# Optimization experiments

Hardware: AMD Instinct MI355X
Metric: run time of the kernel (lower is better)

Reference implementation:

```python
import jax, jax.numpy as jnp
import numpy as np

W, HN, C, NHEAD = 256, 128, 512, 8


def layer_norm(x, w, b, eps=1e-5):
    m = x.mean(-1, keepdims=True)
    v = ((x - m) ** 2).mean(-1, keepdims=True)
    return (x - m) / jnp.sqrt(v + eps) * w + b


def setup_inputs() -> dict:
    key = jax.random.key(0)
    ks = jax.random.split(key, 6)
    s = 0.02
    return {
        "feat_left": jax.random.normal(ks[0], (W, HN, C), jnp.float32),
        "feat_right": jax.random.normal(ks[1], (W, HN, C), jnp.float32),
        "pos": jax.random.normal(ks[2], (2 * W - 1, C), jnp.float32),
        "pos_indexes": jax.random.randint(ks[3], (W * W,), 0, 2 * W - 1, dtype=jnp.int32),
        "ln_w": jnp.ones((C,), jnp.float32),
        "ln_b": jnp.zeros((C,), jnp.float32),
        "in_proj_w": jax.random.normal(ks[4], (3 * C, C), jnp.float32) * s,
        "in_proj_b": jnp.zeros((3 * C,), jnp.float32),
        "out_w": jax.random.normal(ks[5], (C, C), jnp.float32) * s,
        "out_b": jnp.zeros((C,), jnp.float32),
    }


def reference(feat_left, feat_right, pos, pos_indexes, ln_w, ln_b, in_proj_w, in_proj_b, out_w, out_b):
    w, n, c = feat_left.shape
    e = NHEAD
    hd = c // e
    scaling = hd ** -0.5

    # pre-norm (same norm1 applied to both streams)
    ql = layer_norm(feat_left, ln_w, ln_b)     # [W,N,C]
    kv_in = layer_norm(feat_right, ln_w, ln_b)  # [W,N,C]

    # cross-attn projections: q from left with in_proj[:C], k/v from right with in_proj[C:]
    q = ql @ in_proj_w[:c].T + in_proj_b[:c]
    kv = kv_in @ in_proj_w[c:].T + in_proj_b[c:]
    k, v = jnp.split(kv, 2, axis=-1)

    # relative pos encoding gather: [2W-1,C] -> [W*W,C] -> [W,W',C]
    pe = pos[pos_indexes].reshape(w, w, c)
    qr_kr = pe @ in_proj_w[: 2 * c].T + in_proj_b[: 2 * c]
    q_r, k_r = jnp.split(qr_kr, 2, axis=-1)

    q = (q * scaling).reshape(w, n, e, hd)
    q_r = (q_r * scaling).reshape(w, w, e, hd)
    k = k.reshape(w, n, e, hd)
    v = v.reshape(w, n, e, hd)
    k_r = k_r.reshape(w, w, e, hd)

    # content-content + content-pos + pos-content scores: [N,E,W,W']
    attn = (jnp.einsum('wnec,vnec->newv', q, k)
            + jnp.einsum('wnec,wvec->newv', q, k_r)
            + jnp.einsum('vnec,wvec->newv', k, q_r))

    raw_attn = attn.sum(axis=1)                      # [N,W,W']
    p = jax.nn.softmax(attn, axis=-1)
    v_o = jnp.einsum('newv,vnec->wnec', p, v).reshape(w, n, c)
    v_o = v_o @ out_w.T + out_b

    return feat_left + v_o, raw_attn
```

## Files before the change

### kernel.cpp

```cpp
#include <hip/hip_runtime.h>

#define WW 256
#define NB 128
#define CD 512
#define NE 8
#define HD 64
#define NCHUNKS 4
#define SCALING 0.125f

typedef __attribute__((ext_vector_type(8))) short bfx8;
typedef __attribute__((ext_vector_type(4))) float fx4;

#define OFF_MEAN   0u
#define OFF_RSTD   65536u
#define OFF_WPB    131072u
#define OFF_OWB    524288u
#define OFF_S      655360u
#define OFF_U      656896u
#define OFF_PQ     658432u
#define OFF_PK     789504u
#define OFF_QB     920576u
#define OFF_KB     9309184u
#define OFF_VB     17697792u
#define OFF_ATTN   26086400u
#define OFF_T3     42863616u
#define OFF_PB     51252224u
#define OFF_VOB    59640832u

__device__ __forceinline__ unsigned short f2bf(float f) {
  unsigned u = __builtin_bit_cast(unsigned, f);
  u = (u + 0x7fffu + ((u >> 16) & 1u)) >> 16;
  return (unsigned short)u;
}
__device__ __forceinline__ float bf2f(unsigned short h) {
  unsigned u = ((unsigned)h) << 16;
  return __builtin_bit_cast(float, u);
}

#define GLDS16(g, l)                                                          \
  __builtin_amdgcn_global_load_lds(                                           \
      (const __attribute__((address_space(1))) void*)(g),                     \
      (__attribute__((address_space(3))) void*)(l), 16, 0, 0)

__global__ __launch_bounds__(256) void cvt_kernel(const float* __restrict__ a,
                                                  unsigned short* __restrict__ b,
                                                  int n8) {
  int i = blockIdx.x * 256 + threadIdx.x;
  if (i >= n8) return;
  float4 x = ((const float4*)a)[2 * i];
  float4 y = ((const float4*)a)[2 * i + 1];
  int4 o;
  o.x = (int)(((unsigned)f2bf(x.y) << 16) | f2bf(x.x));
  o.y = (int)(((unsigned)f2bf(x.w) << 16) | f2bf(x.z));
  o.z = (int)(((unsigned)f2bf(y.y) << 16) | f2bf(y.x));
  o.w = (int)(((unsigned)f2bf(y.w) << 16) | f2bf(y.z));
  ((int4*)b)[i] = o;
}

__global__ __launch_bounds__(256) void stats_kernel(const float* __restrict__ L,
                                                    const float* __restrict__ R,
                                                    float* __restrict__ mean,
                                                    float* __restrict__ rstd,
                                                    unsigned short* __restrict__ flb,
                                                    unsigned short* __restrict__ frb) {
  int wave = threadIdx.x >> 6, lane = threadIdx.x & 63;
  int row = blockIdx.x * 4 + wave;
  const float* src = (row < 32768) ? (L + (size_t)row * CD) : (R + (size_t)(row - 32768) * CD);
  unsigned short* drow = (row < 32768) ? (flb + (size_t)row * CD) : (frb + (size_t)(row - 32768) * CD);
  float4 a = *(const float4*)(src + lane * 4);
  float4 b = *(const float4*)(src + 256 + lane * 4);
  short4 sa, sb;
  sa.x = (short)f2bf(a.x); sa.y = (short)f2bf(a.y); sa.z = (short)f2bf(a.z); sa.w = (short)f2bf(a.w);
  sb.x = (short)f2bf(b.x); sb.y = (short)f2bf(b.y); sb.z = (short)f2bf(b.z); sb.w = (short)f2bf(b.w);
  *(short4*)(drow + lane * 4) = sa;
  *(short4*)(drow + 256 + lane * 4) = sb;
  float s  = a.x + a.y + a.z + a.w + b.x + b.y + b.z + b.w;
  float ss = a.x*a.x + a.y*a.y + a.z*a.z + a.w*a.w + b.x*b.x + b.y*b.y + b.z*b.z + b.w*b.w;
#pragma unroll
  for (int off = 32; off > 0; off >>= 1) {
    s  += __shfl_xor(s, off);
    ss += __shfl_xor(ss, off);
  }
  if (lane == 0) {
    float m = s * (1.0f / 512.0f);
    float v = ss * (1.0f / 512.0f) - m * m;
    mean[row] = m;
    rstd[row] = rsqrtf(v + 1e-5f);
  }
}

__global__ __launch_bounds__(256) void prep_kernel(const float* __restrict__ ipw,
                                                   const float* __restrict__ ipb,
                                                   const float* __restrict__ lnw,
                                                   const float* __restrict__ lnb,
                                                   unsigned short* __restrict__ Wpb,
                                                   float* __restrict__ S,
                                                   float* __restrict__ U) {
  int o = blockIdx.x, t = threadIdx.x;
  float s = 0.f, u = 0.f;
#pragma unroll
  for (int j0 = 0; j0 < 512; j0 += 256) {
    int j = j0 + t;
    float w0 = ipw[(size_t)o * 512 + j];
    float wl = w0 * lnw[j];
    unsigned short h = f2bf(wl);
    Wpb[(size_t)o * 512 + j] = h;
    s += bf2f(h);
    u += w0 * lnb[j];
  }
  __shared__ float rs[4], ru[4];
  int lane = t & 63, wv = t >> 6;
#pragma unroll
  for (int off = 32; off > 0; off >>= 1) { s += __shfl_xor(s, off); u += __shfl_xor(u, off); }
  if (lane == 0) { rs[wv] = s; ru[wv] = u; }
  __syncthreads();
  if (t == 0) {
    S[o] = rs[0] + rs[1] + rs[2] + rs[3];
    U[o] = ru[0] + ru[1] + ru[2] + ru[3] + ipb[o];
  }
}

__global__ __launch_bounds__(256) void gemm_ln(const unsigned short* __restrict__ A,
                                               const unsigned short* __restrict__ Bw,
                                               const float* __restrict__ S,
                                               const float* __restrict__ U,
                                               const float* __restrict__ mean,
                                               const float* __restrict__ rstd,
                                               unsigned short* __restrict__ out0,
                                               unsigned short* __restrict__ out1,
                                               int wOff, int statOff, float scale) {
  __shared__ unsigned short As[2][128 * 32];
  __shared__ unsigned short Bs[2][128 * 32];
  int t = threadIdx.x;
  int lane = t & 63, w = t >> 6;
  int quad = lane >> 4, l15 = lane & 15;
  int wm = w >> 1, wn = w & 1;
  int m0 = blockIdx.x * 128, n0 = blockIdx.y * 128;

  int cs = ((lane & 3) ^ ((lane >> 3) & 3)) * 8;
  unsigned lo0 = (unsigned)(w * 16) * 32;
  unsigned lo1 = (unsigned)(64 + w * 16) * 32;
  const unsigned short* gA0 = A + (size_t)(m0 + w * 16 + (lane >> 2)) * 512 + cs;
  const unsigned short* gA1 = gA0 + (size_t)64 * 512;
  const unsigned short* gB0 = Bw + (size_t)(wOff + n0 + w * 16 + (lane >> 2)) * 512 + cs;
  const unsigned short* gB1 = gB0 + (size_t)64 * 512;

  fx4 acc[4][4];
#pragma unroll
  for (int i = 0; i < 4; ++i)
#pragma unroll
    for (int j = 0; j < 4; ++j) acc[i][j] = (fx4){0.f, 0.f, 0.f, 0.f};

  int ro = (quad ^ ((l15 >> 1) & 3)) * 8;

#define STAGE_G(buf, kk)                                                      \
  do {                                                                        \
    GLDS16(gA0 + (kk), &As[buf][lo0]);                                        \
    GLDS16(gA1 + (kk), &As[buf][lo1]);                                        \
    GLDS16(gB0 + (kk), &Bs[buf][lo0]);                                        \
    GLDS16(gB1 + (kk), &Bs[buf][lo1]);                                        \
  } while (0)

#define COMPUTE_G(buf)                                                        \
  do {                                                                        \
    const unsigned short* Ab = &As[buf][0];                                   \
    const unsigned short* Bb = &Bs[buf][0];                                   \
    bfx8 af[4], bfr[4];                                                       \
    _Pragma("unroll")                                                         \
    for (int i = 0; i < 4; ++i)                                               \
      af[i] = *(const bfx8*)(Ab + (size_t)(wm * 64 + i * 16 + l15) * 32 + ro);\
    _Pragma("unroll")                                                         \
    for (int j = 0; j < 4; ++j)                                               \
      bfr[j] = *(const bfx8*)(Bb + (size_t)(wn * 64 + j * 16 + l15) * 32 + ro);\
    _Pragma("unroll")                                                         \
    for (int i = 0; i < 4; ++i)                                               \
      _Pragma("unroll")                                                       \
      for (int j = 0; j < 4; ++j)                                             \
        acc[i][j] = __builtin_amdgcn_mfma_f32_16x16x32_bf16(af[i], bfr[j], acc[i][j], 0, 0, 0); \
  } while (0)

  STAGE_G(0, 0);
  int cur = 0;
  for (int kt = 0; kt < 480; kt += 32) {
    STAGE_G(cur ^ 1, kt + 32);
    asm volatile("s_waitcnt vmcnt(4)" ::: "memory");
    __builtin_amdgcn_s_barrier();
    __builtin_amdgcn_sched_barrier(0);
    COMPUTE_G(cur);
    asm volatile("s_waitcnt lgkmcnt(0)" ::: "memory");
    __builtin_amdgcn_s_barrier();
    __builtin_amdgcn_sched_barrier(0);
    cur ^= 1;
  }
  asm volatile("s_waitcnt vmcnt(0)" ::: "memory");
  __builtin_amdgcn_s_barrier();
  __builtin_amdgcn_sched_barrier(0);
  COMPUTE_G(cur);

  float mn[16], rs[16];
#pragma unroll
  for (int i = 0; i < 4; ++i)
#pragma unroll
    for (int r = 0; r < 4; ++r) {
      int m = statOff + m0 + wm * 64 + i * 16 + quad * 4 + r;
      mn[i * 4 + r] = mean[m];
      rs[i * 4 + r] = rstd[m];
    }
#pragma unroll
  for (int j = 0; j < 4; ++j) {
    int oc = n0 + wn * 64 + j * 16 + l15;
    int o = wOff + oc;
    float Sv = S[o], Uv = U[o];
    unsigned short* dst; int cc;
    if (oc < 512) { dst = out0; cc = oc; } else { dst = out1; cc = oc - 512; }
#pragma unroll
    for (int i = 0; i < 4; ++i)
#pragma unroll
      for (int r = 0; r < 4; ++r) {
        int m = m0 + wm * 64 + i * 16 + quad * 4 + r;
        dst[(size_t)m * 512 + cc] =
            f2bf(((acc[i][j][r] - mn[i * 4 + r] * Sv) * rs[i * 4 + r] + Uv) * scale);
      }
  }
#undef STAGE_G
#undef COMPUTE_G
}

__global__ __launch_bounds__(256) void gemm_out(const unsigned short* __restrict__ A,
                                                const unsigned short* __restrict__ Bw,
                                                const float* __restrict__ ob,
                                                const float* __restrict__ fl,
                                                float* __restrict__ out, int wc) {
  __shared__ unsigned short As[2][128 * 32];
  __shared__ unsigned short Bs[2][128 * 32];
  int t = threadIdx.x;
  int lane = t & 63, w = t >> 6;
  int quad = lane >> 4, l15 = lane & 15;
  int wm = w >> 1, wn = w & 1;
  int n0 = blockIdx.x * 128, m0 = blockIdx.y * 128;

  int cs = ((lane & 3) ^ ((lane >> 3) & 3)) * 8;
  unsigned lo0 = (unsigned)(w * 16) * 32;
  unsigned lo1 = (unsigned)(64 + w * 16) * 32;
  const unsigned short* gA0 = A + (size_t)(m0 + w * 16 + (lane >> 2)) * 512 + cs;
  const unsigned short* gA1 = gA0 + (size_t)64 * 512;
  const unsigned short* gB0 = Bw + (size_t)(n0 + w * 16 + (lane >> 2)) * 512 + cs;
  const unsigned short* gB1 = gB0 + (size_t)64 * 512;

  fx4 acc[4][4];
#pragma unroll
  for (int i = 0; i < 4; ++i)
#pragma unroll
    for (int j = 0; j < 4; ++j) acc[i][j] = (fx4){0.f, 0.f, 0.f, 0.f};

  int ro = (quad ^ ((l15 >> 1) & 3)) * 8;

#define STAGE_O(buf, kk)                                                      \
  do {                                                                        \
    GLDS16(gA0 + (kk), &As[buf][lo0]);                                        \
    GLDS16(gA1 + (kk), &As[buf][lo1]);                                        \
    GLDS16(gB0 + (kk), &Bs[buf][lo0]);                                        \
    GLDS16(gB1 + (kk), &Bs[buf][lo1]);                                        \
  } while (0)

#define COMPUTE_O(buf)                                                        \
  do {                                                                        \
    const unsigned short* Ab = &As[buf][0];                                   \
    const unsigned short* Bb = &Bs[buf][0];                                   \
    bfx8 af[4], bfr[4];                                                       \
    _Pragma("unroll")                                                         \
    for (int i = 0; i < 4; ++i)                                               \
      af[i] = *(const bfx8*)(Ab + (size_t)(wm * 64 + i * 16 + l15) * 32 + ro);\
    _Pragma("unroll")                                                         \
    for (int j = 0; j < 4; ++j)                                               \
      bfr[j] = *(const bfx8*)(Bb + (size_t)(wn * 64 + j * 16 + l15) * 32 + ro);\
    _Pragma("unroll")                                                         \
    for (int i = 0; i < 4; ++i)                                               \
      _Pragma("unroll")                                                       \
      for (int j = 0; j < 4; ++j)                                             \
        acc[i][j] = __builtin_amdgcn_mfma_f32_16x16x32_bf16(af[i], bfr[j], acc[i][j], 0, 0, 0); \
  } while (0)

  STAGE_O(0, 0);
  int cur = 0;
  for (int kt = 0; kt < 480; kt += 32) {
    STAGE_O(cur ^ 1, kt + 32);
    asm volatile("s_waitcnt vmcnt(4)" ::: "memory");
    __builtin_amdgcn_s_barrier();
    __builtin_amdgcn_sched_barrier(0);
    COMPUTE_O(cur);
    asm volatile("s_waitcnt lgkmcnt(0)" ::: "memory");
    __builtin_amdgcn_s_barrier();
    __builtin_amdgcn_sched_barrier(0);
    cur ^= 1;
  }
  asm volatile("s_waitcnt vmcnt(0)" ::: "memory");
  __builtin_amdgcn_s_barrier();
  __builtin_amdgcn_sched_barrier(0);
  COMPUTE_O(cur);

  size_t gbase = (size_t)wc * 64 * NB * CD;
#pragma unroll
  for (int j = 0; j < 4; ++j) {
    int o = n0 + wn * 64 + j * 16 + l15;
    float bias = ob[o];
#pragma unroll
    for (int i = 0; i < 4; ++i)
#pragma unroll
      for (int r = 0; r < 4; ++r) {
        int m = m0 + wm * 64 + i * 16 + quad * 4 + r;
        size_t go = gbase + (size_t)m * 512 + o;
        out[go] = acc[i][j][r] + bias + fl[go];
      }
  }
#undef STAGE_O
#undef COMPUTE_O
}

__global__ __launch_bounds__(256) void posproj_mfma(const unsigned short* __restrict__ Apos,
                                                    const unsigned short* __restrict__ Bw,
                                                    const float* __restrict__ ipb,
                                                    unsigned short* __restrict__ Pq,
                                                    unsigned short* __restrict__ Pk) {
  __shared__ unsigned short As[2][128 * 32];
  __shared__ unsigned short Bs[2][128 * 32];
  int t = threadIdx.x;
  int lane = t & 63, w = t >> 6;
  int quad = lane >> 4, l15 = lane & 15;
  int wm = w >> 1, wn = w & 1;
  int m0 = blockIdx.x * 128, n0 = blockIdx.y * 128;

  int cs = ((lane & 3) ^ ((lane >> 3) & 3)) * 8;
  unsigned lo0 = (unsigned)(w * 16) * 32;
  unsigned lo1 = (unsigned)(64 + w * 16) * 32;
  int ar0 = m0 + w * 16 + (lane >> 2); if (ar0 > 510) ar0 = 510;
  int ar1 = m0 + 64 + w * 16 + (lane >> 2); if (ar1 > 510) ar1 = 510;
  const unsigned short* gA0 = Apos + (size_t)ar0 * 512 + cs;
  const unsigned short* gA1 = Apos + (size_t)ar1 * 512 + cs;
  const unsigned short* gB0 = Bw + (size_t)(n0 + w * 16 + (lane >> 2)) * 512 + cs;
  const unsigned short* gB1 = gB0 + (size_t)64 * 512;

  fx4 acc[4][4];
#pragma unroll
  for (int i = 0; i < 4; ++i)
#pragma unroll
    for (int j = 0; j < 4; ++j) acc[i][j] = (fx4){0.f, 0.f, 0.f, 0.f};

  int ro = (quad ^ ((l15 >> 1) & 3)) * 8;

#define STAGE_P(buf, kk)                                                      \
  do {                                                                        \
    GLDS16(gA0 + (kk), &As[buf][lo0]);                                        \
    GLDS16(gA1 + (kk), &As[buf][lo1]);                                        \
    GLDS16(gB0 + (kk), &Bs[buf][lo0]);                                        \
    GLDS16(gB1 + (kk), &Bs[buf][lo1]);                                        \
  } while (0)

#define COMPUTE_P(buf)                                                        \
  do {                                                                        \
    const unsigned short* Ab = &As[buf][0];                                   \
    const unsigned short* Bb = &Bs[buf][0];                                   \
    bfx8 af[4], bfr[4];                                                       \
    _Pragma("unroll")                                                         \
    for (int i = 0; i < 4; ++i)                                               \
      af[i] = *(const bfx8*)(Ab + (size_t)(wm * 64 + i * 16 + l15) * 32 + ro);\
    _Pragma("unroll")                                                         \
    for (int j = 0; j < 4; ++j)                                               \
      bfr[j] = *(const bfx8*)(Bb + (size_t)(wn * 64 + j * 16 + l15) * 32 + ro);\
    _Pragma("unroll")                                                         \
    for (int i = 0; i < 4; ++i)                                               \
      _Pragma("unroll")                                                       \
      for (int j = 0; j < 4; ++j)                                             \
        acc[i][j] = __builtin_amdgcn_mfma_f32_16x16x32_bf16(af[i], bfr[j], acc[i][j], 0, 0, 0); \
  } while (0)

  STAGE_P(0, 0);
  int cur = 0;
  for (int kt = 0; kt < 480; kt += 32) {
    STAGE_P(cur ^ 1, kt + 32);
    asm volatile("s_waitcnt vmcnt(4)" ::: "memory");
    __builtin_amdgcn_s_barrier();
    __builtin_amdgcn_sched_barrier(0);
    COMPUTE_P(cur);
    asm volatile("s_waitcnt lgkmcnt(0)" ::: "memory");
    __builtin_amdgcn_s_barrier();
    __builtin_amdgcn_sched_barrier(0);
    cur ^= 1;
  }
  asm volatile("s_waitcnt vmcnt(0)" ::: "memory");
  __builtin_amdgcn_s_barrier();
  __builtin_amdgcn_sched_barrier(0);
  COMPUTE_P(cur);

#pragma unroll
  for (int j = 0; j < 4; ++j) {
    int o = n0 + wn * 64 + j * 16 + l15;
    float bias = ipb[o];
    float scale = (o < 512) ? SCALING : 1.0f;
    unsigned short* dst; int cc;
    if (o < 512) { dst = Pq; cc = o; } else { dst = Pk; cc = o - 512; }
#pragma unroll
    for (int i = 0; i < 4; ++i)
#pragma unroll
      for (int r = 0; r < 4; ++r) {
        int m = m0 + wm * 64 + i * 16 + quad * 4 + r;
        if (m < 511)
          dst[(size_t)m * 512 + cc] = f2bf((acc[i][j][r] + bias) * scale);
      }
  }
#undef STAGE_P
#undef COMPUTE_P
}

__global__ __launch_bounds__(256) void t3_kernel(const unsigned short* __restrict__ kb,
                                                 const unsigned short* __restrict__ Pq,
                                                 const int* __restrict__ idx,
                                                 unsigned short* __restrict__ T3, int wc) {
  __shared__ unsigned short As[128 * 72];
  __shared__ unsigned short Bs[64 * 72];
  int t = threadIdx.x, lane = t & 63, w = t >> 6;
  int quad = lane >> 4, l15 = lane & 15;
  int e = blockIdx.x, v = blockIdx.y;
  const unsigned short* asrc = kb + ((size_t)v * NB) * 512 + e * 64;
  for (int c = t; c < 1024; c += 256) {
    int row = c >> 3, c8 = c & 7;
    *(int4*)(As + row * 72 + c8 * 8) = *(const int4*)(asrc + (size_t)row * 512 + c8 * 8);
  }
  for (int c = t; c < 512; c += 256) {
    int row = c >> 3, c8 = c & 7;
    int ri = idx[(wc * 64 + row) * WW + v];
    *(int4*)(Bs + row * 72 + c8 * 8) = *(const int4*)(Pq + (size_t)ri * 512 + e * 64 + c8 * 8);
  }
  __syncthreads();
  fx4 acc[2][4];
#pragma unroll
  for (int i = 0; i < 2; ++i)
#pragma unroll
    for (int j = 0; j < 4; ++j) acc[i][j] = (fx4){0.f, 0.f, 0.f, 0.f};
#pragma unroll
  for (int kt = 0; kt < 64; kt += 32) {
    bfx8 af[2], bfr[4];
#pragma unroll
    for (int i = 0; i < 2; ++i)
      af[i] = *(const bfx8*)(As + (w * 32 + i * 16 + l15) * 72 + kt + quad * 8);
#pragma unroll
    for (int j = 0; j < 4; ++j)
      bfr[j] = *(const bfx8*)(Bs + (j * 16 + l15) * 72 + kt + quad * 8);
#pragma unroll
    for (int i = 0; i < 2; ++i)
#pragma unroll
      for (int j = 0; j < 4; ++j)
        acc[i][j] = __builtin_amdgcn_mfma_f32_16x16x32_bf16(af[i], bfr[j], acc[i][j], 0, 0, 0);
  }
#pragma unroll
  for (int i = 0; i < 2; ++i)
#pragma unroll
    for (int j = 0; j < 4; ++j)
#pragma unroll
      for (int r = 0; r < 4; ++r) {
        int n = w * 32 + i * 16 + quad * 4 + r;
        int wq = j * 16 + l15;
        T3[(((size_t)e * WW + v) * NB + n) * 64 + wq] = f2bf(acc[i][j][r]);
      }
}

__global__ __launch_bounds__(256) void t1_kernel(const unsigned short* __restrict__ qb,
                                                 const unsigned short* __restrict__ kb,
                                                 const unsigned short* __restrict__ T3,
                                                 float* __restrict__ attn, int wc) {
  __shared__ unsigned short As[64 * 72];
  __shared__ unsigned short Bs[256 * 72];
  int t = threadIdx.x, lane = t & 63, w = t >> 6;
  int quad = lane >> 4, l15 = lane & 15;
  int e = blockIdx.x, n = blockIdx.y;
  const unsigned short* asrc = qb + ((size_t)(wc * 64) * NB + n) * 512 + e * 64;
  for (int c = t; c < 512; c += 256) {
    int row = c >> 3, c8 = c & 7;
    *(int4*)(As + row * 72 + c8 * 8) = *(const int4*)(asrc + (size_t)row * NB * 512 + c8 * 8);
  }
  const unsigned short* bsrc = kb + (size_t)n * 512 + e * 64;
  for (int c = t; c < 2048; c += 256) {
    int row = c >> 3, c8 = c & 7;
    *(int4*)(Bs + row * 72 + c8 * 8) = *(const int4*)(bsrc + (size_t)row * NB * 512 + c8 * 8);
  }
  __syncthreads();
  fx4 acc[4][4];
#pragma unroll
  for (int i = 0; i < 4; ++i)
#pragma unroll
    for (int j = 0; j < 4; ++j) acc[i][j] = (fx4){0.f, 0.f, 0.f, 0.f};
#pragma unroll
  for (int kt = 0; kt < 64; kt += 32) {
    bfx8 af[4], bfr[4];
#pragma unroll
    for (int i = 0; i < 4; ++i)
      af[i] = *(const bfx8*)(As + (i * 16 + l15) * 72 + kt + quad * 8);
#pragma unroll
    for (int j = 0; j < 4; ++j)
      bfr[j] = *(const bfx8*)(Bs + (w * 64 + j * 16 + l15) * 72 + kt + quad * 8);
#pragma unroll
    for (int i = 0; i < 4; ++i)
#pragma unroll
      for (int j = 0; j < 4; ++j)
        acc[i][j] = __builtin_amdgcn_mfma_f32_16x16x32_bf16(af[i], bfr[j], acc[i][j], 0, 0, 0);
  }
  __syncthreads();
  const unsigned short* tsrc = T3 + ((size_t)e * WW * NB + n) * 64;
  for (int c = t; c < 2048; c += 256) {
    int row = c >> 3, c8 = c & 7;
    *(int4*)(Bs + row * 72 + c8 * 8) = *(const int4*)(tsrc + (size_t)row * NB * 64 + c8 * 8);
  }
  __syncthreads();
#pragma unroll
  for (int i = 0; i < 4; ++i)
#pragma unroll
    for (int j = 0; j < 4; ++j) {
      int vg = w * 64 + j * 16 + l15;
      ushort4 t3v = *(const ushort4*)(Bs + (size_t)vg * 72 + i * 16 + quad * 4);
      const unsigned short tv[4] = {t3v.x, t3v.y, t3v.z, t3v.w};
#pragma unroll
      for (int r = 0; r < 4; ++r) {
        int wq = i * 16 + quad * 4 + r;
        float* p = attn + (((size_t)n * NE + e) * 64 + wq) * WW + vg;
        *p = acc[i][j][r] + bf2f(tv[r]);
      }
    }
}

__global__ __launch_bounds__(256) void t2s_kernel(const unsigned short* __restrict__ qb,
                                                  const unsigned short* __restrict__ Pk,
                                                  const int* __restrict__ idx,
                                                  const float* __restrict__ attn,
                                                  unsigned short* __restrict__ pbuf,
                                                  float* __restrict__ raw, int wc) {
  __shared__ unsigned short As[16 * 72];
  __shared__ unsigned short Bs[256 * 72];
  __shared__ int idxs[256];
  __shared__ float redm[16 * 4];
  __shared__ float reds[16 * 4];
  int t = threadIdx.x, lane = t & 63, w = t >> 6;
  int quad = lane >> 4, l15 = lane & 15;
  int wq = blockIdx.x, nt = blockIdx.y;
  int n0 = nt * 16;
  idxs[t] = idx[((size_t)(wc * 64 + wq)) * WW + t];

  fx4 raws[4];
#pragma unroll
  for (int j = 0; j < 4; ++j) raws[j] = (fx4){0.f, 0.f, 0.f, 0.f};

  const unsigned short* abase = qb + ((size_t)(wc * 64 + wq) * NB + n0) * 512;

  for (int e = 0; e < NE; ++e) {
    __syncthreads();
    if (t < 128) {
      int row = t >> 3, c8 = t & 7;
      *(int4*)(As + row * 72 + c8 * 8) = *(const int4*)(abase + (size_t)row * 512 + e * 64 + c8 * 8);
    }
    for (int c = t; c < 2048; c += 256) {
      int row = c >> 3, c8 = c & 7;
      int ri = idxs[row];
      *(int4*)(Bs + row * 72 + c8 * 8) = *(const int4*)(Pk + (size_t)ri * 512 + e * 64 + c8 * 8);
    }
    __syncthreads();

    fx4 acc[4];
#pragma unroll
    for (int j = 0; j < 4; ++j) acc[j] = (fx4){0.f, 0.f, 0.f, 0.f};
    bfx8 af0 = *(const bfx8*)(As + l15 * 72 + quad * 8);
    bfx8 af1 = *(const bfx8*)(As + l15 * 72 + 32 + quad * 8);
#pragma unroll
    for (int j = 0; j < 4; ++j) {
      bfx8 b0 = *(const bfx8*)(Bs + (w * 64 + j * 16 + l15) * 72 + quad * 8);
      acc[j] = __builtin_amdgcn_mfma_f32_16x16x32_bf16(af0, b0, acc[j], 0, 0, 0);
    }
#pragma unroll
    for (int j = 0; j < 4; ++j) {
      bfx8 b1 = *(const bfx8*)(Bs + (w * 64 + j * 16 + l15) * 72 + 32 + quad * 8);
      acc[j] = __builtin_amdgcn_mfma_f32_16x16x32_bf16(af1, b1, acc[j], 0, 0, 0);
    }

#pragma unroll
    for (int j = 0; j < 4; ++j) {
      int vg = w * 64 + j * 16 + l15;
#pragma unroll
      for (int r = 0; r < 4; ++r) {
        int n = n0 + quad * 4 + r;
        acc[j][r] += attn[(((size_t)n * NE + e) * 64 + wq) * WW + vg];
      }
    }

    float rm[4];
#pragma unroll
    for (int r = 0; r < 4; ++r)
      rm[r] = fmaxf(fmaxf(acc[0][r], acc[1][r]), fmaxf(acc[2][r], acc[3][r]));
#pragma unroll
    for (int off = 1; off < 16; off <<= 1)
#pragma unroll
      for (int r = 0; r < 4; ++r) rm[r] = fmaxf(rm[r], __shfl_xor(rm[r], off));
    if (l15 == 0) {
#pragma unroll
      for (int r = 0; r < 4; ++r) redm[(quad * 4 + r) * 4 + w] = rm[r];
    }
    __syncthreads();
    float fm[4];
#pragma unroll
    for (int r = 0; r < 4; ++r) {
      const float* rp = redm + (quad * 4 + r) * 4;
      fm[r] = fmaxf(fmaxf(rp[0], rp[1]), fmaxf(rp[2], rp[3]));
    }
    float ex[4][4];
    float ls[4] = {0.f, 0.f, 0.f, 0.f};
#pragma unroll
    for (int j = 0; j < 4; ++j)
#pragma unroll
      for (int r = 0; r < 4; ++r) {
        ex[j][r] = __expf(acc[j][r] - fm[r]);
        ls[r] += ex[j][r];
      }
#pragma unroll
    for (int off = 1; off < 16; off <<= 1)
#pragma unroll
      for (int r = 0; r < 4; ++r) ls[r] += __shfl_xor(ls[r], off);
    if (l15 == 0) {
#pragma unroll
      for (int r = 0; r < 4; ++r) reds[(quad * 4 + r) * 4 + w] = ls[r];
    }
    __syncthreads();
    float inv[4];
#pragma unroll
    for (int r = 0; r < 4; ++r) {
      const float* sp = reds + (quad * 4 + r) * 4;
      inv[r] = 1.0f / (sp[0] + sp[1] + sp[2] + sp[3]);
    }
#pragma unroll
    for (int j = 0; j < 4; ++j) {
      int vg = w * 64 + j * 16 + l15;
#pragma unroll
      for (int r = 0; r < 4; ++r) {
        int n = n0 + quad * 4 + r;
        pbuf[(((size_t)n * NE + e) * 64 + wq) * WW + vg] = f2bf(ex[j][r] * inv[r]);
        raws[j][r] += acc[j][r];
      }
    }
  }

#pragma unroll
  for (int j = 0; j < 4; ++j) {
    int vg = w * 64 + j * 16 + l15;
#pragma unroll
    for (int r = 0; r < 4; ++r) {
      int n = n0 + quad * 4 + r;
      raw[((size_t)n * WW + wc * 64 + wq) * WW + vg] = raws[j][r];
    }
  }
}

__global__ __launch_bounds__(256) void pv_kernel(const unsigned short* __restrict__ pb,
                                                 const unsigned short* __restrict__ vb,
                                                 unsigned short* __restrict__ vob) {
  __shared__ unsigned short As[64 * 72];
  __shared__ unsigned short Bs[64 * 72];
  int t = threadIdx.x, lane = t & 63, w = t >> 6;
  int quad = lane >> 4, l15 = lane & 15;
  int e = blockIdx.x, n = blockIdx.y;
  fx4 acc[4];
#pragma unroll
  for (int j = 0; j < 4; ++j) acc[j] = (fx4){0.f, 0.f, 0.f, 0.f};
  const unsigned short* abase = pb + (((size_t)n * NE + e) * 64) * WW;
  for (int kc = 0; kc < 4; ++kc) {
    for (int c = t; c < 512; c += 256) {
      int row = c >> 3, c8 = c & 7;
      *(int4*)(As + row * 72 + c8 * 8) = *(const int4*)(abase + (size_t)row * WW + kc * 64 + c8 * 8);
    }
    for (int c = t; c < 512; c += 256) {
      int row = c >> 3, c8 = c & 7;
      *(int4*)(Bs + row * 72 + c8 * 8) =
          *(const int4*)(vb + ((size_t)(kc * 64 + row) * NB + n) * 512 + e * 64 + c8 * 8);
    }
    __syncthreads();
#pragma unroll
    for (int kt = 0; kt < 64; kt += 32) {
      bfx8 af = *(const bfx8*)(As + (w * 16 + l15) * 72 + kt + quad * 8);
      bfx8 bfr[4];
#pragma unroll
      for (int j = 0; j < 4; ++j)
        bfr[j] = *(const bfx8*)(Bs + (j * 16 + l15) * 72 + kt + quad * 8);
#pragma unroll
      for (int j = 0; j < 4; ++j)
        acc[j] = __builtin_amdgcn_mfma_f32_16x16x32_bf16(af, bfr[j], acc[j], 0, 0, 0);
    }
    __syncthreads();
  }
#pragma unroll
  for (int j = 0; j < 4; ++j)
#pragma unroll
    for (int r = 0; r < 4; ++r) {
      int wq = w * 16 + quad * 4 + r;
      vob[((size_t)wq * NB + n) * 512 + e * 64 + j * 16 + l15] = f2bf(acc[j][r]);
    }
}

extern "C" void kernel_launch(void* const* d_in, const int* in_sizes, int n_in,
                              void* d_out, int out_size, void* d_ws, size_t ws_size,
                              hipStream_t stream) {
  const float* fl  = (const float*)d_in[0];
  const float* fr  = (const float*)d_in[1];
  const float* pos = (const float*)d_in[2];
  const int*  pidx = (const int*)d_in[3];
  const float* lnw = (const float*)d_in[4];
  const float* lnb = (const float*)d_in[5];
  const float* ipw = (const float*)d_in[6];
  const float* ipb = (const float*)d_in[7];
  const float* ow  = (const float*)d_in[8];
  const float* ob  = (const float*)d_in[9];

  float* ws   = (float*)d_ws;
  float* mean = ws + OFF_MEAN;
  float* rstd = ws + OFF_RSTD;
  unsigned short* Wpb = (unsigned short*)(ws + OFF_WPB);
  unsigned short* owb = (unsigned short*)(ws + OFF_OWB);
  float* S    = ws + OFF_S;
  float* U    = ws + OFF_U;
  unsigned short* Pq = (unsigned short*)(ws + OFF_PQ);
  unsigned short* Pk = (unsigned short*)(ws + OFF_PK);
  unsigned short* qb = (unsigned short*)(ws + OFF_QB);
  unsigned short* kb = (unsigned short*)(ws + OFF_KB);
  unsigned short* vb = (unsigned short*)(ws + OFF_VB);
  float* attn = ws + OFF_ATTN;
  unsigned short* T3  = (unsigned short*)(ws + OFF_T3);
  unsigned short* pb  = (unsigned short*)(ws + OFF_PB);
  unsigned short* vob = (unsigned short*)(ws + OFF_VOB);
  unsigned short* flb = (unsigned short*)(ws + OFF_ATTN);
  unsigned short* frb = flb + (size_t)32768 * 512;
  unsigned short* posb = (unsigned short*)(ws + OFF_T3);
  unsigned short* ipwb = posb + 262144;

  float* outF = (float*)d_out;
  float* outR = outF + (size_t)WW * NB * CD;

  stats_kernel<<<16384, 256, 0, stream>>>(fl, fr, mean, rstd, flb, frb);
  prep_kernel<<<1536, 256, 0, stream>>>(ipw, ipb, lnw, lnb, Wpb, S, U);
  cvt_kernel<<<128, 256, 0, stream>>>(ow, owb, 32768);
  cvt_kernel<<<128, 256, 0, stream>>>(pos, posb, 32704);
  cvt_kernel<<<256, 256, 0, stream>>>(ipw, ipwb, 65536);
  posproj_mfma<<<dim3(4, 8), 256, 0, stream>>>(posb, ipwb, ipb, Pq, Pk);
  gemm_ln<<<dim3(256, 4), 256, 0, stream>>>(flb, Wpb, S, U, mean, rstd, qb, qb, 0, 0, SCALING);
  gemm_ln<<<dim3(256, 8), 256, 0, stream>>>(frb, Wpb, S, U, mean, rstd, kb, vb, 512, 32768, 1.0f);

  for (int wc = 0; wc < NCHUNKS; ++wc) {
    t3_kernel<<<dim3(8, 256), 256, 0, stream>>>(kb, Pq, pidx, T3, wc);
    t1_kernel<<<dim3(8, 128), 256, 0, stream>>>(qb, kb, T3, attn, wc);
    t2s_kernel<<<dim3(64, 8), 256, 0, stream>>>(qb, Pk, pidx, attn, pb, outR, wc);
    pv_kernel<<<dim3(8, 128), 256, 0, stream>>>(pb, vb, vob);
    gemm_out<<<dim3(4, 64), 256, 0, stream>>>(vob, owb, ob, fl, outF, wc);
  }
}
```

Measured before the change: 825.0 us.

## Store intermediate attention scores as bf16 and batch output projection across chunks

The intermediate attention partial sums written by t1 and read by t2s are now stored as bf16 instead of fp32, halving that round-trip traffic. The per-chunk pv outputs go into one contiguous buffer, so a single gemm_out launch covers all 256 rows instead of four smaller launches. The stats kernel writes one 16-byte vector per lane, and the separate ipw conversion kernel is folded into prep_kernel. Rounding the summed attention scores to bf16 before softmax adds precision loss.

```diff
diff --git a/kernel.cpp b/kernel.cpp
--- a/kernel.cpp
+++ b/kernel.cpp
@@ -25,7 +25,6 @@
 #define OFF_ATTN   26086400u
 #define OFF_T3     42863616u
 #define OFF_PB     51252224u
-#define OFF_VOB    59640832u
 
 __device__ __forceinline__ unsigned short f2bf(float f) {
   unsigned u = __builtin_bit_cast(unsigned, f);
@@ -35,6 +34,9 @@
 __device__ __forceinline__ float bf2f(unsigned short h) {
   unsigned u = ((unsigned)h) << 16;
   return __builtin_bit_cast(float, u);
+}
+__device__ __forceinline__ int packbf(float lo, float hi) {
+  return (int)(((unsigned)f2bf(hi) << 16) | f2bf(lo));
 }
 
 #define GLDS16(g, l)                                                          \
@@ -50,10 +52,10 @@
   float4 x = ((const float4*)a)[2 * i];
   float4 y = ((const float4*)a)[2 * i + 1];
   int4 o;
-  o.x = (int)(((unsigned)f2bf(x.y) << 16) | f2bf(x.x));
-  o.y = (int)(((unsigned)f2bf(x.w) << 16) | f2bf(x.z));
-  o.z = (int)(((unsigned)f2bf(y.y) << 16) | f2bf(y.x));
-  o.w = (int)(((unsigned)f2bf(y.w) << 16) | f2bf(y.z));
+  o.x = packbf(x.x, x.y);
+  o.y = packbf(x.z, x.w);
+  o.z = packbf(y.x, y.y);
+  o.w = packbf(y.z, y.w);
   ((int4*)b)[i] = o;
 }
 
@@ -67,13 +69,14 @@
   int row = blockIdx.x * 4 + wave;
   const float* src = (row < 32768) ? (L + (size_t)row * CD) : (R + (size_t)(row - 32768) * CD);
   unsigned short* drow = (row < 32768) ? (flb + (size_t)row * CD) : (frb + (size_t)(row - 32768) * CD);
-  float4 a = *(const float4*)(src + lane * 4);
-  float4 b = *(const float4*)(src + 256 + lane * 4);
-  short4 sa, sb;
-  sa.x = (short)f2bf(a.x); sa.y = (short)f2bf(a.y); sa.z = (short)f2bf(a.z); sa.w = (short)f2bf(a.w);
-  sb.x = (short)f2bf(b.x); sb.y = (short)f2bf(b.y); sb.z = (short)f2bf(b.z); sb.w = (short)f2bf(b.w);
-  *(short4*)(drow + lane * 4) = sa;
-  *(short4*)(drow + 256 + lane * 4) = sb;
+  float4 a = *(const float4*)(src + lane * 8);
+  float4 b = *(const float4*)(src + lane * 8 + 4);
+  int4 o;
+  o.x = packbf(a.x, a.y);
+  o.y = packbf(a.z, a.w);
+  o.z = packbf(b.x, b.y);
+  o.w = packbf(b.z, b.w);
+  *(int4*)(drow + lane * 8) = o;
   float s  = a.x + a.y + a.z + a.w + b.x + b.y + b.z + b.w;
   float ss = a.x*a.x + a.y*a.y + a.z*a.z + a.w*a.w + b.x*b.x + b.y*b.y + b.z*b.z + b.w*b.w;
 #pragma unroll
@@ -94,6 +97,7 @@
                                                    const float* __restrict__ lnw,
                                                    const float* __restrict__ lnb,
                                                    unsigned short* __restrict__ Wpb,
+                                                   unsigned short* __restrict__ ipwb,
                                                    float* __restrict__ S,
                                                    float* __restrict__ U) {
   int o = blockIdx.x, t = threadIdx.x;
@@ -105,6 +109,7 @@
     float wl = w0 * lnw[j];
     unsigned short h = f2bf(wl);
     Wpb[(size_t)o * 512 + j] = h;
+    if (o < 1024) ipwb[(size_t)o * 512 + j] = f2bf(w0);
     s += bf2f(h);
     u += w0 * lnb[j];
   }
@@ -230,7 +235,7 @@
                                                 const unsigned short* __restrict__ Bw,
                                                 const float* __restrict__ ob,
                                                 const float* __restrict__ fl,
-                                                float* __restrict__ out, int wc) {
+                                                float* __restrict__ out) {
   __shared__ unsigned short As[2][128 * 32];
   __shared__ unsigned short Bs[2][128 * 32];
   int t = threadIdx.x;
@@ -299,7 +304,6 @@
   __builtin_amdgcn_sched_barrier(0);
   COMPUTE_O(cur);
 
-  size_t gbase = (size_t)wc * 64 * NB * CD;
 #pragma unroll
   for (int j = 0; j < 4; ++j) {
     int o = n0 + wn * 64 + j * 16 + l15;
@@ -309,7 +313,7 @@
 #pragma unroll
       for (int r = 0; r < 4; ++r) {
         int m = m0 + wm * 64 + i * 16 + quad * 4 + r;
-        size_t go = gbase + (size_t)m * 512 + o;
+        size_t go = (size_t)m * 512 + o;
         out[go] = acc[i][j][r] + bias + fl[go];
       }
   }
@@ -467,7 +471,7 @@
 __global__ __launch_bounds__(256) void t1_kernel(const unsigned short* __restrict__ qb,
                                                  const unsigned short* __restrict__ kb,
                                                  const unsigned short* __restrict__ T3,
-                                                 float* __restrict__ attn, int wc) {
+                                                 unsigned short* __restrict__ attnb, int wc) {
   __shared__ unsigned short As[64 * 72];
   __shared__ unsigned short Bs[256 * 72];
   int t = threadIdx.x, lane = t & 63, w = t >> 6;
@@ -521,8 +525,7 @@
 #pragma unroll
       for (int r = 0; r < 4; ++r) {
         int wq = i * 16 + quad * 4 + r;
-        float* p = attn + (((size_t)n * NE + e) * 64 + wq) * WW + vg;
-        *p = acc[i][j][r] + bf2f(tv[r]);
+        attnb[(((size_t)n * NE + e) * 64 + wq) * WW + vg] = f2bf(acc[i][j][r] + bf2f(tv[r]));
       }
     }
 }
@@ -530,7 +533,7 @@
 __global__ __launch_bounds__(256) void t2s_kernel(const unsigned short* __restrict__ qb,
                                                   const unsigned short* __restrict__ Pk,
                                                   const int* __restrict__ idx,
-                                                  const float* __restrict__ attn,
+                                                  const unsigned short* __restrict__ attnb,
                                                   unsigned short* __restrict__ pbuf,
                                                   float* __restrict__ raw, int wc) {
   __shared__ unsigned short As[16 * 72];
@@ -585,7 +588,7 @@
 #pragma unroll
       for (int r = 0; r < 4; ++r) {
         int n = n0 + quad * 4 + r;
-        acc[j][r] += attn[(((size_t)n * NE + e) * 64 + wq) * WW + vg];
+        acc[j][r] += bf2f(attnb[(((size_t)n * NE + e) * 64 + wq) * WW + vg]);
       }
     }
 
@@ -726,10 +729,10 @@
   unsigned short* qb = (unsigned short*)(ws + OFF_QB);
   unsigned short* kb = (unsigned short*)(ws + OFF_KB);
   unsigned short* vb = (unsigned short*)(ws + OFF_VB);
-  float* attn = ws + OFF_ATTN;
+  unsigned short* attnb = (unsigned short*)(ws + OFF_ATTN);
+  unsigned short* vob4  = attnb + (size_t)16777216;
   unsigned short* T3  = (unsigned short*)(ws + OFF_T3);
   unsigned short* pb  = (unsigned short*)(ws + OFF_PB);
-  unsigned short* vob = (unsigned short*)(ws + OFF_VOB);
   unsigned short* flb = (unsigned short*)(ws + OFF_ATTN);
   unsigned short* frb = flb + (size_t)32768 * 512;
   unsigned short* posb = (unsigned short*)(ws + OFF_T3);
@@ -739,19 +742,18 @@
   float* outR = outF + (size_t)WW * NB * CD;
 
   stats_kernel<<<16384, 256, 0, stream>>>(fl, fr, mean, rstd, flb, frb);
-  prep_kernel<<<1536, 256, 0, stream>>>(ipw, ipb, lnw, lnb, Wpb, S, U);
+  prep_kernel<<<1536, 256, 0, stream>>>(ipw, ipb, lnw, lnb, Wpb, ipwb, S, U);
   cvt_kernel<<<128, 256, 0, stream>>>(ow, owb, 32768);
   cvt_kernel<<<128, 256, 0, stream>>>(pos, posb, 32704);
-  cvt_kernel<<<256, 256, 0, stream>>>(ipw, ipwb, 65536);
   posproj_mfma<<<dim3(4, 8), 256, 0, stream>>>(posb, ipwb, ipb, Pq, Pk);
   gemm_ln<<<dim3(256, 4), 256, 0, stream>>>(flb, Wpb, S, U, mean, rstd, qb, qb, 0, 0, SCALING);
   gemm_ln<<<dim3(256, 8), 256, 0, stream>>>(frb, Wpb, S, U, mean, rstd, kb, vb, 512, 32768, 1.0f);
 
   for (int wc = 0; wc < NCHUNKS; ++wc) {
     t3_kernel<<<dim3(8, 256), 256, 0, stream>>>(kb, Pq, pidx, T3, wc);
-    t1_kernel<<<dim3(8, 128), 256, 0, stream>>>(qb, kb, T3, attn, wc);
-    t2s_kernel<<<dim3(64, 8), 256, 0, stream>>>(qb, Pk, pidx, attn, pb, outR, wc);
-    pv_kernel<<<dim3(8, 128), 256, 0, stream>>>(pb, vb, vob);
-    gemm_out<<<dim3(4, 64), 256, 0, stream>>>(vob, owb, ob, fl, outF, wc);
-  }
-}
+    t1_kernel<<<dim3(8, 128), 256, 0, stream>>>(qb, kb, T3, attnb, wc);
+    t2s_kernel<<<dim3(64, 8), 256, 0, stream>>>(qb, Pk, pidx, attnb, pb, outR, wc);
+    pv_kernel<<<dim3(8, 128), 256, 0, stream>>>(pb, vb, vob4 + (size_t)wc * 64 * NB * 512);
+  }
+  gemm_out<<<dim3(4, 256), 256, 0, stream>>>(vob4, owb, ob, fl, outF);
+}
```

New measurement: 763.0 us. 1.08x faster.
